# Optimization experiments

Measured on AMD Instinct MI355X. Metric: run time of the kernel, lower is better.

The kernel has to match this reference:

```python
import jax, jax.numpy as jnp
import numpy as np

N_NODES = 25000
N_EDGES = 250000
IN_DIM = 256
HID = 128
HEADS = 2
NEG_SLOPE_ATT = 0.2   # PyG GATConv default negative_slope
NEG_SLOPE_ACT = 0.01  # F.leaky_relu default


def setup_inputs() -> dict:
    key = jax.random.key(0)
    ks = jax.random.split(key, 8)
    x = jax.random.normal(ks[0], (N_NODES, IN_DIM), dtype=jnp.float32)
    edge_index = jax.random.randint(ks[1], (2, N_EDGES), 0, N_NODES, dtype=jnp.int32)
    # GATConv params: lin weight [heads*out, in], att vectors [heads, out], bias [heads*out]
    s = 1.0 / np.sqrt(IN_DIM)
    W = jax.random.uniform(ks[2], (HEADS * HID, IN_DIM), jnp.float32, -s, s)
    att_src = jax.random.uniform(ks[3], (HEADS, HID), jnp.float32, -s, s)
    att_dst = jax.random.uniform(ks[4], (HEADS, HID), jnp.float32, -s, s)
    bias = jnp.zeros((HEADS * HID,), jnp.float32)
    s2 = 1.0 / np.sqrt(HEADS * HID * 2)
    fc1_w = jax.random.uniform(ks[5], (3, HEADS * HID * 2), jnp.float32, -s2, s2)
    fc1_b = jax.random.uniform(ks[6], (3,), jnp.float32, -s2, s2)
    return {"x": x, "edge_index": edge_index, "W": W, "att_src": att_src,
            "att_dst": att_dst, "bias": bias, "fc1_w": fc1_w, "fc1_b": fc1_b}


def _gat_conv(x, edge_index, W, att_src, att_dst, bias):
    N = x.shape[0]
    h = (x @ W.T).reshape(N, HEADS, HID)             # [N,H,C]
    a_src = jnp.einsum('nhc,hc->nh', h, att_src)     # [N,H]
    a_dst = jnp.einsum('nhc,hc->nh', h, att_dst)
    # add self loops (PyG GATConv default)
    loops = jnp.arange(N, dtype=edge_index.dtype)
    src = jnp.concatenate([edge_index[0], loops])
    dst = jnp.concatenate([edge_index[1], loops])
    e = jax.nn.leaky_relu(a_src[src] + a_dst[dst], NEG_SLOPE_ATT)  # [E+N,H]
    # scatter-softmax over destination nodes
    m = jax.ops.segment_max(e, dst, num_segments=N)
    ex = jnp.exp(e - m[dst])
    z = jax.ops.segment_sum(ex, dst, num_segments=N)
    alpha = ex / z[dst]                              # [E+N,H]
    msg = alpha[:, :, None] * h[src]                 # [E+N,H,C]
    out = jax.ops.segment_sum(msg, dst, num_segments=N)  # [N,H,C]
    return out.reshape(N, HEADS * HID) + bias


def reference(x, edge_index, W, att_src, att_dst, bias, fc1_w, fc1_b):
    # dropout is identity in eval mode
    h = _gat_conv(x, edge_index, W, att_src, att_dst, bias)
    h = jax.nn.leaky_relu(h, NEG_SLOPE_ACT)
    edge_rep = jnp.concatenate([h[edge_index[0]], h[edge_index[1]]], axis=1)  # [E, 4*HID]
    return edge_rep @ fc1_w.T + fc1_b               # [E, 3]
```

## Files before the change

kernel.cpp:

```cpp
#include <hip/hip_runtime.h>
#include <hip/hip_bf16.h>

#define N_NODES 25000
#define N_EDGES 250000
#define N_TOT   275000
#define FDIM    256
#define NB_SCAN 98
#define M_PAD   25024

typedef __attribute__((ext_vector_type(8))) short bf16x8;
typedef __attribute__((ext_vector_type(4))) float f32x4;

__device__ inline float bf2f(unsigned short s) {
    union { unsigned u; float f; } v; v.u = ((unsigned)s) << 16;
    return v.f;
}

__global__ void k_deg(const int* __restrict__ ei, int* __restrict__ deg) {
    int i = blockIdx.x * 256 + threadIdx.x;
    if (i < N_EDGES) atomicAdd(&deg[ei[N_EDGES + i]], 1);
}

__global__ __launch_bounds__(512) void k_gemm(const float* __restrict__ x,
                                              const float* __restrict__ W,
                                              const float* __restrict__ att_src,
                                              const float* __restrict__ att_dst,
                                              __hip_bfloat16* __restrict__ hb,
                                              float* __restrict__ a_src,
                                              float* __restrict__ a_dst) {
    __shared__ char lds[40960];
    __shared__ float s_as[64][2];
    __shared__ float s_ad[64][2];
    const int m0   = blockIdx.x * 64;
    const int t    = threadIdx.x;
    const int lane = t & 63;
    const int wid  = t >> 6;
    const int wr   = wid >> 2;
    const int wc   = wid & 3;
    if (t < 256) {
        s_as[t >> 2][t & 1] = 0.f;
        s_ad[t >> 2][t & 1] = 0.f;
    }
    f32x4 acc[2][4];
    #pragma unroll
    for (int mi = 0; mi < 2; ++mi)
        #pragma unroll
        for (int ni = 0; ni < 4; ++ni)
            acc[mi][ni] = (f32x4){0.f, 0.f, 0.f, 0.f};

    for (int kc = 0; kc < 256; kc += 64) {
        __syncthreads();
        #pragma unroll
        for (int q = 0; q < 2; ++q) {
            int fi = q * 512 + t;
            int row = fi >> 4, ks4 = fi & 15;
            int node = m0 + row;
            f32x4 v = (f32x4){0.f, 0.f, 0.f, 0.f};
            if (node < N_NODES) v = *reinterpret_cast<const f32x4*>(x + node * 256 + kc + ks4 * 4);
            __hip_bfloat16 b[4];
            b[0] = __float2bfloat16(v.x); b[1] = __float2bfloat16(v.y);
            b[2] = __float2bfloat16(v.z); b[3] = __float2bfloat16(v.w);
            int byte = (row * 128 + ks4 * 8) ^ ((row & 7) << 4);
            *reinterpret_cast<ushort4*>(lds + byte) = *reinterpret_cast<const ushort4*>(b);
        }
        #pragma unroll
        for (int q = 0; q < 8; ++q) {
            int fi = q * 512 + t;
            int col = fi >> 4, ks4 = fi & 15;
            f32x4 v = *reinterpret_cast<const f32x4*>(W + col * 256 + kc + ks4 * 4);
            __hip_bfloat16 b[4];
            b[0] = __float2bfloat16(v.x); b[1] = __float2bfloat16(v.y);
            b[2] = __float2bfloat16(v.z); b[3] = __float2bfloat16(v.w);
            int byte = 8192 + ((col * 128 + ks4 * 8) ^ ((col & 7) << 4));
            *reinterpret_cast<ushort4*>(lds + byte) = *reinterpret_cast<const ushort4*>(b);
        }
        __syncthreads();
        #pragma unroll
        for (int ks = 0; ks < 2; ++ks) {
            bf16x8 a[2], b[4];
            #pragma unroll
            for (int mi = 0; mi < 2; ++mi) {
                int row = wr * 32 + mi * 16 + (lane & 15);
                int byte = (row * 128 + ks * 64 + (lane >> 4) * 16) ^ ((row & 7) << 4);
                a[mi] = *reinterpret_cast<const bf16x8*>(lds + byte);
            }
            #pragma unroll
            for (int ni = 0; ni < 4; ++ni) {
                int col = wc * 64 + ni * 16 + (lane & 15);
                int byte = 8192 + ((col * 128 + ks * 64 + (lane >> 4) * 16) ^ ((col & 7) << 4));
                b[ni] = *reinterpret_cast<const bf16x8*>(lds + byte);
            }
            #pragma unroll
            for (int mi = 0; mi < 2; ++mi)
                #pragma unroll
                for (int ni = 0; ni < 4; ++ni)
                    acc[mi][ni] = __builtin_amdgcn_mfma_f32_16x16x32_bf16(
                        a[mi], b[ni], acc[mi][ni], 0, 0, 0);
        }
    }
    #pragma unroll
    for (int mi = 0; mi < 2; ++mi)
        #pragma unroll
        for (int r = 0; r < 4; ++r) {
            int row = m0 + wr * 32 + mi * 16 + (lane >> 4) * 4 + r;
            #pragma unroll
            for (int ni = 0; ni < 4; ++ni) {
                int col = wc * 64 + ni * 16 + (lane & 15);
                hb[row * 256 + col] = __float2bfloat16(acc[mi][ni][r]);
            }
        }
    const int hd0 = wc >> 1;
    float as_[4], ad_[4];
    #pragma unroll
    for (int ni = 0; ni < 4; ++ni) {
        int col = wc * 64 + ni * 16 + (lane & 15);
        as_[ni] = att_src[col];
        ad_[ni] = att_dst[col];
    }
    #pragma unroll
    for (int mi = 0; mi < 2; ++mi)
        #pragma unroll
        for (int r = 0; r < 4; ++r) {
            float ps = acc[mi][0][r] * as_[0] + acc[mi][1][r] * as_[1]
                     + acc[mi][2][r] * as_[2] + acc[mi][3][r] * as_[3];
            float pd = acc[mi][0][r] * ad_[0] + acc[mi][1][r] * ad_[1]
                     + acc[mi][2][r] * ad_[2] + acc[mi][3][r] * ad_[3];
            #pragma unroll
            for (int o = 8; o > 0; o >>= 1) {
                ps += __shfl_down(ps, o);
                pd += __shfl_down(pd, o);
            }
            if ((lane & 15) == 0) {
                int rl = wr * 32 + mi * 16 + (lane >> 4) * 4 + r;
                atomicAdd(&s_as[rl][hd0], ps);
                atomicAdd(&s_ad[rl][hd0], pd);
            }
        }
    __syncthreads();
    if (t < 128) {
        int rl = t >> 1, hd = t & 1;
        int row = m0 + rl;
        if (row < N_NODES) {
            a_src[row * 2 + hd] = s_as[rl][hd];
            a_dst[row * 2 + hd] = s_ad[rl][hd];
        }
    }
}

__global__ __launch_bounds__(256) void k_scan1(const int* __restrict__ deg,
                                               int* __restrict__ offs,
                                               int* __restrict__ bsum) {
    __shared__ int sh[256];
    int b = blockIdx.x, t = threadIdx.x;
    int i = b * 256 + t;
    int v = (i < N_NODES) ? (deg[i] + 1) : 0;
    sh[t] = v;
    __syncthreads();
    #pragma unroll
    for (int o = 1; o < 256; o <<= 1) {
        int u = (t >= o) ? sh[t - o] : 0;
        __syncthreads();
        sh[t] += u;
        __syncthreads();
    }
    int incl = sh[t];
    if (i < N_NODES) offs[i] = incl - v;
    if (t == 255) bsum[b] = incl;
}

__global__ __launch_bounds__(128) void k_scan2(int* __restrict__ bsum) {
    __shared__ int sh[128];
    int t = threadIdx.x;
    int v = (t < NB_SCAN) ? bsum[t] : 0;
    sh[t] = v;
    __syncthreads();
    #pragma unroll
    for (int o = 1; o < 128; o <<= 1) {
        int u = (t >= o) ? sh[t - o] : 0;
        __syncthreads();
        sh[t] += u;
        __syncthreads();
    }
    if (t < NB_SCAN) bsum[t] = sh[t] - v;
}

__global__ __launch_bounds__(256) void k_scan3(int* __restrict__ offs,
                                               const int* __restrict__ bsum,
                                               int* __restrict__ cursor) {
    int i = blockIdx.x * 256 + threadIdx.x;
    if (i < N_NODES) {
        int o = offs[i] + bsum[i >> 8];
        offs[i]   = o;
        cursor[i] = o;
    }
}

__global__ void k_csr_fill(const int* __restrict__ ei,
                           const float* __restrict__ a_src,
                           const float* __restrict__ a_dst,
                           int* __restrict__ cursor,
                           float4* __restrict__ csr) {
    int i = blockIdx.x * 256 + threadIdx.x;
    if (i >= N_TOT) return;
    int src, dst;
    if (i < N_EDGES) { src = ei[i]; dst = ei[N_EDGES + i]; }
    else             { src = dst = i - N_EDGES; }
    float2 as = *reinterpret_cast<const float2*>(a_src + src * 2);
    float2 ad = *reinterpret_cast<const float2*>(a_dst + dst * 2);
    float v0 = as.x + ad.x;
    float v1 = as.y + ad.y;
    v0 = v0 > 0.f ? v0 : 0.2f * v0;
    v1 = v1 > 0.f ? v1 : 0.2f * v1;
    int pos = atomicAdd(&cursor[dst], 1);
    float4 r;
    r.x = __int_as_float(src);
    r.y = expf(v0);
    r.z = expf(v1);
    r.w = 0.f;
    csr[pos] = r;
}

__global__ __launch_bounds__(256) void k_node_aggregate(const float4* __restrict__ csr,
                                                        const int* __restrict__ offs,
                                                        const int* __restrict__ deg,
                                                        const unsigned short* __restrict__ hb,
                                                        const float* __restrict__ bias,
                                                        const float* __restrict__ fc1_w,
                                                        const float* __restrict__ fc1_b,
                                                        float* __restrict__ p_src,
                                                        float* __restrict__ p_dst) {
    const int n = (blockIdx.x << 2) + (threadIdx.x >> 6);
    const int lane = threadIdx.x & 63;
    if (n >= N_NODES) return;
    const int s = offs[n];
    const int e = s + deg[n] + 1;
    f32x4 acc0 = (f32x4){0.f, 0.f, 0.f, 0.f};
    f32x4 acc1 = (f32x4){0.f, 0.f, 0.f, 0.f};
    float zs0 = 0.f, zs1 = 0.f;
    int it = s;
    for (; it + 2 <= e; it += 2) {
        float4 r0 = csr[it], r1 = csr[it + 1];
        int s0 = __float_as_int(r0.x), s1 = __float_as_int(r1.x);
        float w0 = lane < 32 ? r0.y : r0.z;
        float w1 = lane < 32 ? r1.y : r1.z;
        ushort4 h0 = *reinterpret_cast<const ushort4*>(hb + s0 * FDIM + lane * 4);
        ushort4 h1 = *reinterpret_cast<const ushort4*>(hb + s1 * FDIM + lane * 4);
        acc0.x += w0 * bf2f(h0.x); acc0.y += w0 * bf2f(h0.y);
        acc0.z += w0 * bf2f(h0.z); acc0.w += w0 * bf2f(h0.w);
        acc1.x += w1 * bf2f(h1.x); acc1.y += w1 * bf2f(h1.y);
        acc1.z += w1 * bf2f(h1.z); acc1.w += w1 * bf2f(h1.w);
        zs0 += w0; zs1 += w1;
    }
    if (it < e) {
        float4 r0 = csr[it];
        int s0 = __float_as_int(r0.x);
        float w0 = lane < 32 ? r0.y : r0.z;
        ushort4 h0 = *reinterpret_cast<const ushort4*>(hb + s0 * FDIM + lane * 4);
        acc0.x += w0 * bf2f(h0.x); acc0.y += w0 * bf2f(h0.y);
        acc0.z += w0 * bf2f(h0.z); acc0.w += w0 * bf2f(h0.w);
        zs0 += w0;
    }
    const float inv = 1.f / (zs0 + zs1);
    f32x4 bv = *reinterpret_cast<const f32x4*>(bias + lane * 4);
    float h2_0 = (acc0.x + acc1.x) * inv + bv.x;
    float h2_1 = (acc0.y + acc1.y) * inv + bv.y;
    float h2_2 = (acc0.z + acc1.z) * inv + bv.z;
    float h2_3 = (acc0.w + acc1.w) * inv + bv.w;
    h2_0 = h2_0 > 0.f ? h2_0 : 0.01f * h2_0;
    h2_1 = h2_1 > 0.f ? h2_1 : 0.01f * h2_1;
    h2_2 = h2_2 > 0.f ? h2_2 : 0.01f * h2_2;
    h2_3 = h2_3 > 0.f ? h2_3 : 0.01f * h2_3;
    f32x4 wa0 = *reinterpret_cast<const f32x4*>(fc1_w + 0 * 512 + lane * 4);
    f32x4 wa1 = *reinterpret_cast<const f32x4*>(fc1_w + 1 * 512 + lane * 4);
    f32x4 wa2 = *reinterpret_cast<const f32x4*>(fc1_w + 2 * 512 + lane * 4);
    f32x4 wb0 = *reinterpret_cast<const f32x4*>(fc1_w + 0 * 512 + 256 + lane * 4);
    f32x4 wb1 = *reinterpret_cast<const f32x4*>(fc1_w + 1 * 512 + 256 + lane * 4);
    f32x4 wb2 = *reinterpret_cast<const f32x4*>(fc1_w + 2 * 512 + 256 + lane * 4);
    float v0 = wa0.x * h2_0 + wa0.y * h2_1 + wa0.z * h2_2 + wa0.w * h2_3;
    float v1 = wa1.x * h2_0 + wa1.y * h2_1 + wa1.z * h2_2 + wa1.w * h2_3;
    float v2 = wa2.x * h2_0 + wa2.y * h2_1 + wa2.z * h2_2 + wa2.w * h2_3;
    float v3 = wb0.x * h2_0 + wb0.y * h2_1 + wb0.z * h2_2 + wb0.w * h2_3;
    float v4 = wb1.x * h2_0 + wb1.y * h2_1 + wb1.z * h2_2 + wb1.w * h2_3;
    float v5 = wb2.x * h2_0 + wb2.y * h2_1 + wb2.z * h2_2 + wb2.w * h2_3;
    #pragma unroll
    for (int o = 32; o > 0; o >>= 1) {
        v0 += __shfl_down(v0, o); v1 += __shfl_down(v1, o); v2 += __shfl_down(v2, o);
        v3 += __shfl_down(v3, o); v4 += __shfl_down(v4, o); v5 += __shfl_down(v5, o);
    }
    if (lane == 0) {
        f32x4 ps = (f32x4){v0 + fc1_b[0], v1 + fc1_b[1], v2 + fc1_b[2], 0.f};
        f32x4 pd = (f32x4){v3, v4, v5, 0.f};
        *reinterpret_cast<f32x4*>(p_src + n * 4) = ps;
        *reinterpret_cast<f32x4*>(p_dst + n * 4) = pd;
    }
}

__global__ void k_edge_out(const int* __restrict__ ei,
                           const float* __restrict__ p_src,
                           const float* __restrict__ p_dst,
                           float* __restrict__ out) {
    int i = blockIdx.x * 256 + threadIdx.x;
    if (i >= N_EDGES) return;
    int s = ei[i], d = ei[N_EDGES + i];
    f32x4 ps = *reinterpret_cast<const f32x4*>(p_src + s * 4);
    f32x4 pd = *reinterpret_cast<const f32x4*>(p_dst + d * 4);
    out[i * 3 + 0] = ps.x + pd.x;
    out[i * 3 + 1] = ps.y + pd.y;
    out[i * 3 + 2] = ps.z + pd.z;
}

extern "C" void kernel_launch(void* const* d_in, const int* in_sizes, int n_in,
                              void* d_out, int out_size, void* d_ws, size_t ws_size,
                              hipStream_t stream) {
    const float* x       = (const float*)d_in[0];
    const int*   ei      = (const int*)d_in[1];
    const float* W       = (const float*)d_in[2];
    const float* att_src = (const float*)d_in[3];
    const float* att_dst = (const float*)d_in[4];
    const float* bias    = (const float*)d_in[5];
    const float* fc1_w   = (const float*)d_in[6];
    const float* fc1_b   = (const float*)d_in[7];
    float* out = (float*)d_out;

    float4* csr = (float4*)d_ws;
    __hip_bfloat16* hb = (__hip_bfloat16*)(csr + N_TOT);
    float* a_src = (float*)(hb + M_PAD * FDIM);
    float* a_dst = a_src + 2 * N_NODES;
    float* p_src = a_dst + 2 * N_NODES;
    float* p_dst = p_src + 4 * N_NODES;
    int* deg     = (int*)(p_dst + 4 * N_NODES);
    int* offs    = deg + N_NODES;
    int* cursor  = offs + N_NODES;
    int* bsum    = cursor + N_NODES;

    hipMemsetAsync(deg, 0, N_NODES * sizeof(int), stream);
    k_deg<<<(N_EDGES + 255) / 256, 256, 0, stream>>>(ei, deg);
    k_gemm<<<(M_PAD / 64), 512, 0, stream>>>(x, W, att_src, att_dst, hb, a_src, a_dst);
    k_scan1<<<NB_SCAN, 256, 0, stream>>>(deg, offs, bsum);
    k_scan2<<<1, 128, 0, stream>>>(bsum);
    k_scan3<<<NB_SCAN, 256, 0, stream>>>(offs, bsum, cursor);
    k_csr_fill<<<(N_TOT + 255) / 256, 256, 0, stream>>>(ei, a_src, a_dst, cursor, csr);
    k_node_aggregate<<<(N_NODES + 3) / 4, 256, 0, stream>>>(
        csr, offs, deg, (const unsigned short*)hb, bias, fc1_w, fc1_b, p_src, p_dst);
    k_edge_out<<<(N_EDGES + 255) / 256, 256, 0, stream>>>(ei, p_src, p_dst, out);
}
```

Baseline: 165.7 us.

## Fuse degree count into GEMM, single-block scan, unroll aggregate, vectorize edge output

After: 199.4 us. +20.4%, slower.

```diff
diff --git a/kernel.cpp b/kernel.cpp
--- a/kernel.cpp
+++ b/kernel.cpp
@@ -5,8 +5,8 @@
 #define N_EDGES 250000
 #define N_TOT   275000
 #define FDIM    256
-#define NB_SCAN 98
 #define M_PAD   25024
+#define GEMM_THREADS (391 * 512)
 
 typedef __attribute__((ext_vector_type(8))) short bf16x8;
 typedef __attribute__((ext_vector_type(4))) float f32x4;
@@ -16,18 +16,15 @@
     return v.f;
 }
 
-__global__ void k_deg(const int* __restrict__ ei, int* __restrict__ deg) {
-    int i = blockIdx.x * 256 + threadIdx.x;
-    if (i < N_EDGES) atomicAdd(&deg[ei[N_EDGES + i]], 1);
-}
-
 __global__ __launch_bounds__(512) void k_gemm(const float* __restrict__ x,
                                               const float* __restrict__ W,
+                                              const int* __restrict__ ei,
                                               const float* __restrict__ att_src,
                                               const float* __restrict__ att_dst,
                                               __hip_bfloat16* __restrict__ hb,
                                               float* __restrict__ a_src,
-                                              float* __restrict__ a_dst) {
+                                              float* __restrict__ a_dst,
+                                              int* __restrict__ deg) {
     __shared__ char lds[40960];
     __shared__ float s_as[64][2];
     __shared__ float s_ad[64][2];
@@ -37,6 +34,10 @@
     const int wid  = t >> 6;
     const int wr   = wid >> 2;
     const int wc   = wid & 3;
+
+    for (int i = blockIdx.x * 512 + t; i < N_EDGES; i += GEMM_THREADS)
+        atomicAdd(&deg[ei[N_EDGES + i]], 1);
+
     if (t < 256) {
         s_as[t >> 2][t & 1] = 0.f;
         s_ad[t >> 2][t & 1] = 0.f;
@@ -147,51 +148,29 @@
     }
 }
 
-__global__ __launch_bounds__(256) void k_scan1(const int* __restrict__ deg,
+__global__ __launch_bounds__(1024) void k_scan(const int* __restrict__ deg,
                                                int* __restrict__ offs,
-                                               int* __restrict__ bsum) {
-    __shared__ int sh[256];
-    int b = blockIdx.x, t = threadIdx.x;
-    int i = b * 256 + t;
-    int v = (i < N_NODES) ? (deg[i] + 1) : 0;
-    sh[t] = v;
+                                               int* __restrict__ cursor) {
+    __shared__ int sh[1024];
+    const int t = threadIdx.x;
+    const int i0 = t * 25;
+    const int i1 = (i0 + 25 < N_NODES) ? i0 + 25 : N_NODES;
+    int tot = 0;
+    for (int i = i0; i < i1; ++i) tot += deg[i] + 1;
+    sh[t] = tot;
     __syncthreads();
     #pragma unroll
-    for (int o = 1; o < 256; o <<= 1) {
+    for (int o = 1; o < 1024; o <<= 1) {
         int u = (t >= o) ? sh[t - o] : 0;
         __syncthreads();
         sh[t] += u;
         __syncthreads();
     }
-    int incl = sh[t];
-    if (i < N_NODES) offs[i] = incl - v;
-    if (t == 255) bsum[b] = incl;
-}
-
-__global__ __launch_bounds__(128) void k_scan2(int* __restrict__ bsum) {
-    __shared__ int sh[128];
-    int t = threadIdx.x;
-    int v = (t < NB_SCAN) ? bsum[t] : 0;
-    sh[t] = v;
-    __syncthreads();
-    #pragma unroll
-    for (int o = 1; o < 128; o <<= 1) {
-        int u = (t >= o) ? sh[t - o] : 0;
-        __syncthreads();
-        sh[t] += u;
-        __syncthreads();
-    }
-    if (t < NB_SCAN) bsum[t] = sh[t] - v;
-}
-
-__global__ __launch_bounds__(256) void k_scan3(int* __restrict__ offs,
-                                               const int* __restrict__ bsum,
-                                               int* __restrict__ cursor) {
-    int i = blockIdx.x * 256 + threadIdx.x;
-    if (i < N_NODES) {
-        int o = offs[i] + bsum[i >> 8];
-        offs[i]   = o;
-        cursor[i] = o;
+    int run = sh[t] - tot;
+    for (int i = i0; i < i1; ++i) {
+        offs[i] = run;
+        cursor[i] = run;
+        run += deg[i] + 1;
     }
 }
 
@@ -236,22 +215,33 @@
     const int e = s + deg[n] + 1;
     f32x4 acc0 = (f32x4){0.f, 0.f, 0.f, 0.f};
     f32x4 acc1 = (f32x4){0.f, 0.f, 0.f, 0.f};
-    float zs0 = 0.f, zs1 = 0.f;
+    f32x4 acc2 = (f32x4){0.f, 0.f, 0.f, 0.f};
+    f32x4 acc3 = (f32x4){0.f, 0.f, 0.f, 0.f};
+    float zs0 = 0.f, zs1 = 0.f, zs2 = 0.f, zs3 = 0.f;
     int it = s;
-    for (; it + 2 <= e; it += 2) {
-        float4 r0 = csr[it], r1 = csr[it + 1];
+    for (; it + 4 <= e; it += 4) {
+        float4 r0 = csr[it], r1 = csr[it + 1], r2 = csr[it + 2], r3 = csr[it + 3];
         int s0 = __float_as_int(r0.x), s1 = __float_as_int(r1.x);
+        int s2 = __float_as_int(r2.x), s3 = __float_as_int(r3.x);
         float w0 = lane < 32 ? r0.y : r0.z;
         float w1 = lane < 32 ? r1.y : r1.z;
+        float w2 = lane < 32 ? r2.y : r2.z;
+        float w3 = lane < 32 ? r3.y : r3.z;
         ushort4 h0 = *reinterpret_cast<const ushort4*>(hb + s0 * FDIM + lane * 4);
         ushort4 h1 = *reinterpret_cast<const ushort4*>(hb + s1 * FDIM + lane * 4);
+        ushort4 h2 = *reinterpret_cast<const ushort4*>(hb + s2 * FDIM + lane * 4);
+        ushort4 h3 = *reinterpret_cast<const ushort4*>(hb + s3 * FDIM + lane * 4);
         acc0.x += w0 * bf2f(h0.x); acc0.y += w0 * bf2f(h0.y);
         acc0.z += w0 * bf2f(h0.z); acc0.w += w0 * bf2f(h0.w);
         acc1.x += w1 * bf2f(h1.x); acc1.y += w1 * bf2f(h1.y);
         acc1.z += w1 * bf2f(h1.z); acc1.w += w1 * bf2f(h1.w);
-        zs0 += w0; zs1 += w1;
-    }
-    if (it < e) {
+        acc2.x += w2 * bf2f(h2.x); acc2.y += w2 * bf2f(h2.y);
+        acc2.z += w2 * bf2f(h2.z); acc2.w += w2 * bf2f(h2.w);
+        acc3.x += w3 * bf2f(h3.x); acc3.y += w3 * bf2f(h3.y);
+        acc3.z += w3 * bf2f(h3.z); acc3.w += w3 * bf2f(h3.w);
+        zs0 += w0; zs1 += w1; zs2 += w2; zs3 += w3;
+    }
+    for (; it < e; ++it) {
         float4 r0 = csr[it];
         int s0 = __float_as_int(r0.x);
         float w0 = lane < 32 ? r0.y : r0.z;
@@ -260,12 +250,12 @@
         acc0.z += w0 * bf2f(h0.z); acc0.w += w0 * bf2f(h0.w);
         zs0 += w0;
     }
-    const float inv = 1.f / (zs0 + zs1);
+    const float inv = 1.f / ((zs0 + zs1) + (zs2 + zs3));
     f32x4 bv = *reinterpret_cast<const f32x4*>(bias + lane * 4);
-    float h2_0 = (acc0.x + acc1.x) * inv + bv.x;
-    float h2_1 = (acc0.y + acc1.y) * inv + bv.y;
-    float h2_2 = (acc0.z + acc1.z) * inv + bv.z;
-    float h2_3 = (acc0.w + acc1.w) * inv + bv.w;
+    float h2_0 = ((acc0.x + acc1.x) + (acc2.x + acc3.x)) * inv + bv.x;
+    float h2_1 = ((acc0.y + acc1.y) + (acc2.y + acc3.y)) * inv + bv.y;
+    float h2_2 = ((acc0.z + acc1.z) + (acc2.z + acc3.z)) * inv + bv.z;
+    float h2_3 = ((acc0.w + acc1.w) + (acc2.w + acc3.w)) * inv + bv.w;
     h2_0 = h2_0 > 0.f ? h2_0 : 0.01f * h2_0;
     h2_1 = h2_1 > 0.f ? h2_1 : 0.01f * h2_1;
     h2_2 = h2_2 > 0.f ? h2_2 : 0.01f * h2_2;
@@ -299,14 +289,23 @@
                            const float* __restrict__ p_src,
                            const float* __restrict__ p_dst,
                            float* __restrict__ out) {
-    int i = blockIdx.x * 256 + threadIdx.x;
-    if (i >= N_EDGES) return;
-    int s = ei[i], d = ei[N_EDGES + i];
-    f32x4 ps = *reinterpret_cast<const f32x4*>(p_src + s * 4);
-    f32x4 pd = *reinterpret_cast<const f32x4*>(p_dst + d * 4);
-    out[i * 3 + 0] = ps.x + pd.x;
-    out[i * 3 + 1] = ps.y + pd.y;
-    out[i * 3 + 2] = ps.z + pd.z;
+    int i0 = (blockIdx.x * 256 + threadIdx.x) * 4;
+    if (i0 >= N_EDGES) return;
+    int4 sv = *reinterpret_cast<const int4*>(ei + i0);
+    int4 dv = *reinterpret_cast<const int4*>(ei + N_EDGES + i0);
+    f32x4 p0 = *reinterpret_cast<const f32x4*>(p_src + sv.x * 4);
+    f32x4 p1 = *reinterpret_cast<const f32x4*>(p_src + sv.y * 4);
+    f32x4 p2 = *reinterpret_cast<const f32x4*>(p_src + sv.z * 4);
+    f32x4 p3 = *reinterpret_cast<const f32x4*>(p_src + sv.w * 4);
+    f32x4 q0 = *reinterpret_cast<const f32x4*>(p_dst + dv.x * 4);
+    f32x4 q1 = *reinterpret_cast<const f32x4*>(p_dst + dv.y * 4);
+    f32x4 q2 = *reinterpret_cast<const f32x4*>(p_dst + dv.z * 4);
+    f32x4 q3 = *reinterpret_cast<const f32x4*>(p_dst + dv.w * 4);
+    f32x4 o0 = (f32x4){p0.x + q0.x, p0.y + q0.y, p0.z + q0.z, p1.x + q1.x};
+    f32x4 o1 = (f32x4){p1.y + q1.y, p1.z + q1.z, p2.x + q2.x, p2.y + q2.y};
+    f32x4 o2 = (f32x4){p2.z + q2.z, p3.x + q3.x, p3.y + q3.y, p3.z + q3.z};
+    f32x4* op = reinterpret_cast<f32x4*>(out + i0 * 3);
+    op[0] = o0; op[1] = o1; op[2] = o2;
 }
 
 extern "C" void kernel_launch(void* const* d_in, const int* in_sizes, int n_in,
@@ -331,16 +330,13 @@
     int* deg     = (int*)(p_dst + 4 * N_NODES);
     int* offs    = deg + N_NODES;
     int* cursor  = offs + N_NODES;
-    int* bsum    = cursor + N_NODES;
 
     hipMemsetAsync(deg, 0, N_NODES * sizeof(int), stream);
-    k_deg<<<(N_EDGES + 255) / 256, 256, 0, stream>>>(ei, deg);
-    k_gemm<<<(M_PAD / 64), 512, 0, stream>>>(x, W, att_src, att_dst, hb, a_src, a_dst);
-    k_scan1<<<NB_SCAN, 256, 0, stream>>>(deg, offs, bsum);
-    k_scan2<<<1, 128, 0, stream>>>(bsum);
-    k_scan3<<<NB_SCAN, 256, 0, stream>>>(offs, bsum, cursor);
+    k_gemm<<<(M_PAD / 64), 512, 0, stream>>>(x, W, ei, att_src, att_dst, hb,
+                                             a_src, a_dst, deg);
+    k_scan<<<1, 1024, 0, stream>>>(deg, offs, cursor);
     k_csr_fill<<<(N_TOT + 255) / 256, 256, 0, stream>>>(ei, a_src, a_dst, cursor, csr);
     k_node_aggregate<<<(N_NODES + 3) / 4, 256, 0, stream>>>(
         csr, offs, deg, (const unsigned short*)hb, bias, fc1_w, fc1_b, p_src, p_dst);
-    k_edge_out<<<(N_EDGES + 255) / 256, 256, 0, stream>>>(ei, p_src, p_dst, out);
-}
+    k_edge_out<<<(N_EDGES / 4 + 255) / 256, 256, 0, stream>>>(ei, p_src, p_dst, out);
+}
```
